# Optimization experiments

Measured on AMD Instinct MI355X. Metric: run time of the kernel, lower is better.

Reference implementation:

```python
import jax, jax.numpy as jnp
import numpy as np

NUM_DAYOFWEEK, NUM_TIME, NUM_MONTH, NUM_DAY = 7, 24, 12, 31
NUM_DESTINATION = 100000
NUM_FACTOR = 128
NUM_DIM = NUM_FACTOR // 4  # 32
N = 1048576


def setup_inputs() -> dict:
    key = jax.random.key(0)
    ks = jax.random.split(key, 10)
    std = 0.1
    return {
        "dayofweek": jax.random.randint(ks[0], (N,), 0, NUM_DAYOFWEEK),
        "time": jax.random.randint(ks[1], (N,), 0, NUM_TIME),
        "month": jax.random.randint(ks[2], (N,), 0, NUM_MONTH),
        "day": jax.random.randint(ks[3], (N,), 0, NUM_DAY),
        "destination": jax.random.randint(ks[4], (N,), 0, NUM_DESTINATION),
        "W_dayofweek": std * jax.random.normal(ks[5], (NUM_DAYOFWEEK, NUM_DIM), dtype=jnp.float32),
        "W_time": std * jax.random.normal(ks[6], (NUM_TIME, NUM_DIM), dtype=jnp.float32),
        "W_month": std * jax.random.normal(ks[7], (NUM_MONTH, NUM_DIM), dtype=jnp.float32),
        "W_day": std * jax.random.normal(ks[8], (NUM_DAY, NUM_DIM), dtype=jnp.float32),
        "W_item": std * jax.random.normal(ks[9], (NUM_DESTINATION, NUM_FACTOR), dtype=jnp.float32),
    }


def reference(dayofweek, time, month, day, destination,
              W_dayofweek, W_time, W_month, W_day, W_item) -> jnp.ndarray:
    # Gather per-feature embeddings and concat into user vector [N, num_factor]
    user = jnp.concatenate([
        W_dayofweek[dayofweek],  # [N, 32]
        W_time[time],            # [N, 32]
        W_month[month],          # [N, 32]
        W_day[day],              # [N, 32]
    ], axis=-1)
    item = W_item[destination]   # [N, 128]
    # Original: diagonal(mm(user, item.T)) == rowwise dot product; compute it directly.
    return jnp.sum(user * item, axis=-1)  # [N]
```

## Files before the change

### kernel.cpp

```cpp
#include <hip/hip_runtime.h>


constexpr int NDIM = 32;
constexpr int SZ_DOW = 7 * NDIM, SZ_TIM = 24 * NDIM, SZ_MON = 12 * NDIM, SZ_DAY = 31 * NDIM;
constexpr int B_DOW = 0;
constexpr int B_TIM = B_DOW + SZ_DOW;
constexpr int B_MON = B_TIM + SZ_TIM;
constexpr int B_DAY = B_MON + SZ_MON;
constexpr int TAB_TOT = B_DAY + SZ_DAY;

constexpr int NB   = 32;
constexpr int DDIV = 3125;
constexpr int NBLK = 256;
constexpr int SPB  = 4096;

typedef unsigned long long u64;

__global__ __launch_bounds__(256)
void bin_kernel(const int* __restrict__ dow, const int* __restrict__ tim,
                const int* __restrict__ mon, const int* __restrict__ day,
                const int* __restrict__ dest,
                int* __restrict__ cntG, int* __restrict__ lbaseG,
                u64* __restrict__ payload, unsigned short* __restrict__ invl, int n)
{
    __shared__ u64 stage[SPB];
    __shared__ unsigned short ist[SPB];
    __shared__ int hist[NB], lbase[NB], cursor[NB];

    const int t = threadIdx.x, b = blockIdx.x;
    const int g0 = b * SPB;
    const int rem = n - g0;
    const int len = rem < SPB ? rem : SPB;

    int dreg[16];
#pragma unroll
    for (int i = 0; i < 16; i++) {
        const int k = i * 256 + t;
        dreg[i] = (k < len) ? dest[g0 + k] : -1;
    }
    if (t < NB) hist[t] = 0;
    __syncthreads();
#pragma unroll
    for (int i = 0; i < 16; i++)
        if (dreg[i] >= 0) atomicAdd(&hist[dreg[i] / DDIV], 1);
    __syncthreads();
    if (t == 0) {
        int run = 0;
        for (int q = 0; q < NB; q++) { lbase[q] = run; run += hist[q]; }
    }
    __syncthreads();
    if (t < NB) { cursor[t] = lbase[t]; cntG[b * NB + t] = hist[t]; lbaseG[b * NB + t] = lbase[t]; }
    __syncthreads();
#pragma unroll
    for (int i = 0; i < 16; i++) {
        const int k = i * 256 + t;
        if (k < len) {
            const int ds = dreg[i];
            const int q  = ds / DDIV;
            const int j  = atomicAdd(&cursor[q], 1);
            const u64 p = (u64)(unsigned)(g0 + k)
                | ((u64)(unsigned)ds          << 20)
                | ((u64)(unsigned)dow[g0 + k] << 37)
                | ((u64)(unsigned)tim[g0 + k] << 40)
                | ((u64)(unsigned)mon[g0 + k] << 45)
                | ((u64)(unsigned)day[g0 + k] << 49);
            stage[j] = p;
            ist[k] = (unsigned short)j;
        }
    }
    __syncthreads();
#pragma unroll
    for (int i = 0; i < 16; i++) {
        const int k = i * 256 + t;
        if (k < len) {
            payload[g0 + k] = stage[k];
            if (invl) invl[g0 + k] = ist[k];
        }
    }
}

__global__ __launch_bounds__(256, 4)
void mf_main_kernel(const u64* __restrict__ payload,
                    const float* __restrict__ Wdow, const float* __restrict__ Wtim,
                    const float* __restrict__ Wmon, const float* __restrict__ Wday,
                    const float* __restrict__ Witem,
                    const int* __restrict__ cntG, const int* __restrict__ lbaseG,
                    float* __restrict__ res, float* __restrict__ out)
{
    __shared__ float tab[TAB_TOT];
    const int tid = threadIdx.x;
    for (int i = tid; i < SZ_DOW; i += 256) tab[B_DOW + i] = Wdow[i];
    for (int i = tid; i < SZ_TIM; i += 256) tab[B_TIM + i] = Wtim[i];
    for (int i = tid; i < SZ_MON; i += 256) tab[B_MON + i] = Wmon[i];
    for (int i = tid; i < SZ_DAY; i += 256) tab[B_DAY + i] = Wday[i];
    __syncthreads();

    const int sub = tid & 63;
    const int wv  = tid >> 6;
    const int g   = sub >> 3;
    const int l8  = sub & 7;
    const int col = l8 * 4;
    const int tb[4] = {B_DOW, B_TIM, B_MON, B_DAY};
    const int sh[4] = {37, 40, 45, 49};
    const int mk[4] = {7, 31, 15, 31};

    const int x = blockIdx.x & 7;
    const int s = blockIdx.x >> 3;

    for (int p = 0; p < 4; p++) {
        const int q  = x + 8 * p;
        const int L  = cntG[s * NB + q];
        const int st = s * SPB + lbaseG[s * NB + q];

        for (int i = wv * 16; i < L; i += 64) {
            const int i0 = i + g, i1 = i + 8 + g;
            const bool v0 = i0 < L, v1 = i1 < L;

            const u64 p0 = v0 ? payload[st + i0] : 0ull;
            const u64 p1 = v1 ? payload[st + i1] : 0ull;

            const int id0 = (int)(p0 & 0xFFFFFull), d0 = (int)((p0 >> 20) & 0x1FFFFull);
            const int id1 = (int)(p1 & 0xFFFFFull), d1 = (int)((p1 >> 20) & 0x1FFFFull);

            const float* r0 = Witem + (long)d0 * 128 + col;
            const float* r1 = Witem + (long)d1 * 128 + col;

            float4 it0[4], it1[4], us0[4], us1[4];
#pragma unroll
            for (int j = 0; j < 4; j++) it0[j] = *reinterpret_cast<const float4*>(r0 + j * NDIM);
#pragma unroll
            for (int j = 0; j < 4; j++) it1[j] = *reinterpret_cast<const float4*>(r1 + j * NDIM);
#pragma unroll
            for (int j = 0; j < 4; j++) {
                const int idx = (int)((p0 >> sh[j]) & (u64)mk[j]);
                us0[j] = *reinterpret_cast<const float4*>(&tab[tb[j] + idx * NDIM + col]);
            }
#pragma unroll
            for (int j = 0; j < 4; j++) {
                const int idx = (int)((p1 >> sh[j]) & (u64)mk[j]);
                us1[j] = *reinterpret_cast<const float4*>(&tab[tb[j] + idx * NDIM + col]);
            }

            float a0 = 0.f, a1 = 0.f;
#pragma unroll
            for (int j = 0; j < 4; j++) {
                a0 += it0[j].x * us0[j].x + it0[j].y * us0[j].y
                    + it0[j].z * us0[j].z + it0[j].w * us0[j].w;
                a1 += it1[j].x * us1[j].x + it1[j].y * us1[j].y
                    + it1[j].z * us1[j].z + it1[j].w * us1[j].w;
            }

            a0 += __shfl_xor(a0, 1);  a1 += __shfl_xor(a1, 1);
            a0 += __shfl_xor(a0, 2);  a1 += __shfl_xor(a1, 2);
            a0 += __shfl_xor(a0, 4);  a1 += __shfl_xor(a1, 4);

            if (l8 == 0) {
                if (res) {
                    if (v0) res[st + i0] = a0;
                    if (v1) res[st + i1] = a1;
                } else {
                    if (v0) out[id0] = a0;
                    if (v1) out[id1] = a1;
                }
            }
        }
    }
}

__global__ __launch_bounds__(256)
void unperm_kernel(const float* __restrict__ res, const unsigned short* __restrict__ invl,
                   float* __restrict__ out, int n)
{
    __shared__ float r[SPB];
    const int t = threadIdx.x, b = blockIdx.x;
    const int g0 = b * SPB;
    const int rem = n - g0;
    const int len = rem < SPB ? rem : SPB;
#pragma unroll
    for (int i = 0; i < 16; i++) {
        const int k = i * 256 + t;
        if (k < len) r[k] = res[g0 + k];
    }
    __syncthreads();
#pragma unroll
    for (int i = 0; i < 16; i++) {
        const int k = i * 256 + t;
        if (k < len) out[g0 + k] = r[invl[g0 + k]];
    }
}

__global__ __launch_bounds__(256, 8)
void mf_dot_kernel(const int* __restrict__ dow, const int* __restrict__ tim,
                   const int* __restrict__ mon, const int* __restrict__ day,
                   const int* __restrict__ dest,
                   const float* __restrict__ Wdow, const float* __restrict__ Wtim,
                   const float* __restrict__ Wmon, const float* __restrict__ Wday,
                   const float* __restrict__ Witem,
                   float* __restrict__ out, int n_samples)
{
    __shared__ float tab[TAB_TOT];
    const int tid = threadIdx.x;
    for (int i = tid; i < SZ_DOW; i += 256) tab[B_DOW + i] = Wdow[i];
    for (int i = tid; i < SZ_TIM; i += 256) tab[B_TIM + i] = Wtim[i];
    for (int i = tid; i < SZ_MON; i += 256) tab[B_MON + i] = Wmon[i];
    for (int i = tid; i < SZ_DAY; i += 256) tab[B_DAY + i] = Wday[i];
    __syncthreads();
    const int lane = tid & 63, sub = lane & 31, wave = tid >> 6, half = lane >> 5;
    const int t = sub >> 3, dofs = (sub & 7) * 4;
    const int* idxp  = (t == 0) ? dow   : (t == 1) ? tim   : (t == 2) ? mon   : day;
    const int  tbase = (t == 0) ? B_DOW : (t == 1) ? B_TIM : (t == 2) ? B_MON : B_DAY;
    long n = (long)blockIdx.x * 8 + wave * 2 + half;
    const long stride = (long)gridDim.x * 8;
    for (; n < n_samples; n += stride) {
        const int idx = idxp[n];
        const int ds  = dest[n];
        const float4 u  = *reinterpret_cast<const float4*>(&tab[tbase + idx * NDIM + dofs]);
        const float4 it = *reinterpret_cast<const float4*>(&Witem[(long)ds * 128 + sub * 4]);
        float r = u.x * it.x + u.y * it.y + u.z * it.z + u.w * it.w;
        r += __shfl_xor(r, 16); r += __shfl_xor(r, 8); r += __shfl_xor(r, 4);
        r += __shfl_xor(r, 2);  r += __shfl_xor(r, 1);
        if (sub == 0) out[n] = r;
    }
}

extern "C" void kernel_launch(void* const* d_in, const int* in_sizes, int n_in,
                              void* d_out, int out_size, void* d_ws, size_t ws_size,
                              hipStream_t stream)
{
    const int*   dow   = (const int*)d_in[0];
    const int*   tim   = (const int*)d_in[1];
    const int*   mon   = (const int*)d_in[2];
    const int*   day   = (const int*)d_in[3];
    const int*   dest  = (const int*)d_in[4];
    const float* Wdow  = (const float*)d_in[5];
    const float* Wtim  = (const float*)d_in[6];
    const float* Wmon  = (const float*)d_in[7];
    const float* Wday  = (const float*)d_in[8];
    const float* Witem = (const float*)d_in[9];
    float* out = (float*)d_out;

    const int n = in_sizes[0];
    const int cap = NBLK * SPB;

    const size_t off_payload = 64 * 1024;
    const size_t off_invl    = off_payload + (size_t)cap * 8;
    const size_t off_res     = off_invl + (size_t)cap * 2;
    const size_t need_full   = off_res + (size_t)cap * 4;
    const size_t need_mid    = off_invl;

    if ((size_t)ws_size < need_mid || n > cap) {
        hipLaunchKernelGGL(mf_dot_kernel, dim3(2048), dim3(256), 0, stream,
                           dow, tim, mon, day, dest,
                           Wdow, Wtim, Wmon, Wday, Witem, out, n);
        return;
    }

    const bool full = (size_t)ws_size >= need_full;

    int* cntG   = (int*)d_ws;
    int* lbaseG = (int*)((char*)d_ws + 32 * 1024);
    u64* payload = (u64*)((char*)d_ws + off_payload);
    unsigned short* invl = full ? (unsigned short*)((char*)d_ws + off_invl) : nullptr;
    float* res           = full ? (float*)((char*)d_ws + off_res) : nullptr;

    hipLaunchKernelGGL(bin_kernel, dim3(NBLK), dim3(256), 0, stream,
                       dow, tim, mon, day, dest, cntG, lbaseG, payload, invl, n);
    hipLaunchKernelGGL(mf_main_kernel, dim3(2048), dim3(256), 0, stream,
                       payload, Wdow, Wtim, Wmon, Wday, Witem, cntG, lbaseG, res, out);
    if (full)
        hipLaunchKernelGGL(unperm_kernel, dim3(NBLK), dim3(256), 0, stream,
                           res, invl, out, n);
}
```

Measured before the change: 167.8 us.

## Halve bin segment size, pad LDS table rows, prefetch indices in bin kernel

Segments shrink from 4096 to 2048 samples, which doubles the bin and unperm block count and gives the main kernel 4096 blocks with higher occupancy bounds. The user-embedding table in LDS is padded to a row stride of 36 floats to reduce bank conflicts on the float4 reads. The bin kernel loads the four small index arrays together with dest and packs them early, instead of loading them inside the atomic scatter loop. The partial-workspace path is removed, so the three-kernel pipeline now needs the full workspace or falls back to the direct kernel. Smaller segments also mean fewer samples per destination bucket and more per-block overhead.

```diff
diff --git a/kernel.cpp b/kernel.cpp
--- a/kernel.cpp
+++ b/kernel.cpp
@@ -2,21 +2,32 @@
 
 
 constexpr int NDIM = 32;
-constexpr int SZ_DOW = 7 * NDIM, SZ_TIM = 24 * NDIM, SZ_MON = 12 * NDIM, SZ_DAY = 31 * NDIM;
+constexpr int TS   = 36;
+constexpr int R_DOW = 7, R_TIM = 24, R_MON = 12, R_DAY = 31;
 constexpr int B_DOW = 0;
-constexpr int B_TIM = B_DOW + SZ_DOW;
-constexpr int B_MON = B_TIM + SZ_TIM;
-constexpr int B_DAY = B_MON + SZ_MON;
-constexpr int TAB_TOT = B_DAY + SZ_DAY;
+constexpr int B_TIM = B_DOW + R_DOW * TS;
+constexpr int B_MON = B_TIM + R_TIM * TS;
+constexpr int B_DAY = B_MON + R_MON * TS;
+constexpr int TAB_TOT = B_DAY + R_DAY * TS;
 
 constexpr int NB   = 32;
 constexpr int DDIV = 3125;
-constexpr int NBLK = 256;
-constexpr int SPB  = 4096;
+constexpr int NBLK = 512;
+constexpr int SPB  = 2048;
+constexpr int IPT  = SPB / 256;
 
 typedef unsigned long long u64;
 
-__global__ __launch_bounds__(256)
+__device__ __forceinline__ void load_tab(float* tab, const float* Wdow, const float* Wtim,
+                                         const float* Wmon, const float* Wday) {
+    const int t = threadIdx.x;
+    for (int i = t; i < R_DOW * NDIM; i += 256) tab[B_DOW + (i >> 5) * TS + (i & 31)] = Wdow[i];
+    for (int i = t; i < R_TIM * NDIM; i += 256) tab[B_TIM + (i >> 5) * TS + (i & 31)] = Wtim[i];
+    for (int i = t; i < R_MON * NDIM; i += 256) tab[B_MON + (i >> 5) * TS + (i & 31)] = Wmon[i];
+    for (int i = t; i < R_DAY * NDIM; i += 256) tab[B_DAY + (i >> 5) * TS + (i & 31)] = Wday[i];
+}
+
+__global__ __launch_bounds__(256, 2)
 void bin_kernel(const int* __restrict__ dow, const int* __restrict__ tim,
                 const int* __restrict__ mon, const int* __restrict__ day,
                 const int* __restrict__ dest,
@@ -32,16 +43,20 @@
     const int rem = n - g0;
     const int len = rem < SPB ? rem : SPB;
 
-    int dreg[16];
-#pragma unroll
-    for (int i = 0; i < 16; i++) {
-        const int k = i * 256 + t;
-        dreg[i] = (k < len) ? dest[g0 + k] : -1;
+    int dreg[IPT], pkreg[IPT];
+#pragma unroll
+    for (int i = 0; i < IPT; i++) {
+        const int k = i * 256 + t;
+        if (k < len) {
+            const int idx = g0 + k;
+            dreg[i]  = dest[idx];
+            pkreg[i] = dow[idx] | (tim[idx] << 3) | (mon[idx] << 8) | (day[idx] << 12);
+        } else { dreg[i] = -1; pkreg[i] = 0; }
     }
     if (t < NB) hist[t] = 0;
     __syncthreads();
 #pragma unroll
-    for (int i = 0; i < 16; i++)
+    for (int i = 0; i < IPT; i++)
         if (dreg[i] >= 0) atomicAdd(&hist[dreg[i] / DDIV], 1);
     __syncthreads();
     if (t == 0) {
@@ -52,49 +67,41 @@
     if (t < NB) { cursor[t] = lbase[t]; cntG[b * NB + t] = hist[t]; lbaseG[b * NB + t] = lbase[t]; }
     __syncthreads();
 #pragma unroll
-    for (int i = 0; i < 16; i++) {
+    for (int i = 0; i < IPT; i++) {
         const int k = i * 256 + t;
         if (k < len) {
             const int ds = dreg[i];
-            const int q  = ds / DDIV;
-            const int j  = atomicAdd(&cursor[q], 1);
-            const u64 p = (u64)(unsigned)(g0 + k)
-                | ((u64)(unsigned)ds          << 20)
-                | ((u64)(unsigned)dow[g0 + k] << 37)
-                | ((u64)(unsigned)tim[g0 + k] << 40)
-                | ((u64)(unsigned)mon[g0 + k] << 45)
-                | ((u64)(unsigned)day[g0 + k] << 49);
-            stage[j] = p;
+            const int j  = atomicAdd(&cursor[ds / DDIV], 1);
+            stage[j] = (u64)(unsigned)(g0 + k)
+                     | ((u64)(unsigned)ds       << 20)
+                     | ((u64)(unsigned)pkreg[i] << 37);
             ist[k] = (unsigned short)j;
         }
     }
     __syncthreads();
 #pragma unroll
-    for (int i = 0; i < 16; i++) {
+    for (int i = 0; i < IPT; i++) {
         const int k = i * 256 + t;
         if (k < len) {
             payload[g0 + k] = stage[k];
-            if (invl) invl[g0 + k] = ist[k];
+            invl[g0 + k]    = ist[k];
         }
     }
 }
 
-__global__ __launch_bounds__(256, 4)
+__global__ __launch_bounds__(256, 8)
 void mf_main_kernel(const u64* __restrict__ payload,
                     const float* __restrict__ Wdow, const float* __restrict__ Wtim,
                     const float* __restrict__ Wmon, const float* __restrict__ Wday,
                     const float* __restrict__ Witem,
                     const int* __restrict__ cntG, const int* __restrict__ lbaseG,
-                    float* __restrict__ res, float* __restrict__ out)
+                    float* __restrict__ res)
 {
     __shared__ float tab[TAB_TOT];
+    load_tab(tab, Wdow, Wtim, Wmon, Wday);
+    __syncthreads();
+
     const int tid = threadIdx.x;
-    for (int i = tid; i < SZ_DOW; i += 256) tab[B_DOW + i] = Wdow[i];
-    for (int i = tid; i < SZ_TIM; i += 256) tab[B_TIM + i] = Wtim[i];
-    for (int i = tid; i < SZ_MON; i += 256) tab[B_MON + i] = Wmon[i];
-    for (int i = tid; i < SZ_DAY; i += 256) tab[B_DAY + i] = Wday[i];
-    __syncthreads();
-
     const int sub = tid & 63;
     const int wv  = tid >> 6;
     const int g   = sub >> 3;
@@ -119,8 +126,8 @@
             const u64 p0 = v0 ? payload[st + i0] : 0ull;
             const u64 p1 = v1 ? payload[st + i1] : 0ull;
 
-            const int id0 = (int)(p0 & 0xFFFFFull), d0 = (int)((p0 >> 20) & 0x1FFFFull);
-            const int id1 = (int)(p1 & 0xFFFFFull), d1 = (int)((p1 >> 20) & 0x1FFFFull);
+            const int d0 = (int)((p0 >> 20) & 0x1FFFFull);
+            const int d1 = (int)((p1 >> 20) & 0x1FFFFull);
 
             const float* r0 = Witem + (long)d0 * 128 + col;
             const float* r1 = Witem + (long)d1 * 128 + col;
@@ -133,12 +140,12 @@
 #pragma unroll
             for (int j = 0; j < 4; j++) {
                 const int idx = (int)((p0 >> sh[j]) & (u64)mk[j]);
-                us0[j] = *reinterpret_cast<const float4*>(&tab[tb[j] + idx * NDIM + col]);
+                us0[j] = *reinterpret_cast<const float4*>(&tab[tb[j] + idx * TS + col]);
             }
 #pragma unroll
             for (int j = 0; j < 4; j++) {
                 const int idx = (int)((p1 >> sh[j]) & (u64)mk[j]);
-                us1[j] = *reinterpret_cast<const float4*>(&tab[tb[j] + idx * NDIM + col]);
+                us1[j] = *reinterpret_cast<const float4*>(&tab[tb[j] + idx * TS + col]);
             }
 
             float a0 = 0.f, a1 = 0.f;
@@ -155,19 +162,14 @@
             a0 += __shfl_xor(a0, 4);  a1 += __shfl_xor(a1, 4);
 
             if (l8 == 0) {
-                if (res) {
-                    if (v0) res[st + i0] = a0;
-                    if (v1) res[st + i1] = a1;
-                } else {
-                    if (v0) out[id0] = a0;
-                    if (v1) out[id1] = a1;
-                }
+                if (v0) res[st + i0] = a0;
+                if (v1) res[st + i1] = a1;
             }
         }
     }
 }
 
-__global__ __launch_bounds__(256)
+__global__ __launch_bounds__(256, 2)
 void unperm_kernel(const float* __restrict__ res, const unsigned short* __restrict__ invl,
                    float* __restrict__ out, int n)
 {
@@ -177,13 +179,13 @@
     const int rem = n - g0;
     const int len = rem < SPB ? rem : SPB;
 #pragma unroll
-    for (int i = 0; i < 16; i++) {
+    for (int i = 0; i < IPT; i++) {
         const int k = i * 256 + t;
         if (k < len) r[k] = res[g0 + k];
     }
     __syncthreads();
 #pragma unroll
-    for (int i = 0; i < 16; i++) {
+    for (int i = 0; i < IPT; i++) {
         const int k = i * 256 + t;
         if (k < len) out[g0 + k] = r[invl[g0 + k]];
     }
@@ -199,12 +201,9 @@
                    float* __restrict__ out, int n_samples)
 {
     __shared__ float tab[TAB_TOT];
+    load_tab(tab, Wdow, Wtim, Wmon, Wday);
+    __syncthreads();
     const int tid = threadIdx.x;
-    for (int i = tid; i < SZ_DOW; i += 256) tab[B_DOW + i] = Wdow[i];
-    for (int i = tid; i < SZ_TIM; i += 256) tab[B_TIM + i] = Wtim[i];
-    for (int i = tid; i < SZ_MON; i += 256) tab[B_MON + i] = Wmon[i];
-    for (int i = tid; i < SZ_DAY; i += 256) tab[B_DAY + i] = Wday[i];
-    __syncthreads();
     const int lane = tid & 63, sub = lane & 31, wave = tid >> 6, half = lane >> 5;
     const int t = sub >> 3, dofs = (sub & 7) * 4;
     const int* idxp  = (t == 0) ? dow   : (t == 1) ? tim   : (t == 2) ? mon   : day;
@@ -214,7 +213,7 @@
     for (; n < n_samples; n += stride) {
         const int idx = idxp[n];
         const int ds  = dest[n];
-        const float4 u  = *reinterpret_cast<const float4*>(&tab[tbase + idx * NDIM + dofs]);
+        const float4 u  = *reinterpret_cast<const float4*>(&tab[tbase + idx * TS + dofs]);
         const float4 it = *reinterpret_cast<const float4*>(&Witem[(long)ds * 128 + sub * 4]);
         float r = u.x * it.x + u.y * it.y + u.z * it.z + u.w * it.w;
         r += __shfl_xor(r, 16); r += __shfl_xor(r, 8); r += __shfl_xor(r, 4);
@@ -242,32 +241,28 @@
     const int n = in_sizes[0];
     const int cap = NBLK * SPB;
 
-    const size_t off_payload = 64 * 1024;
+    const size_t off_payload = 128 * 1024;
     const size_t off_invl    = off_payload + (size_t)cap * 8;
     const size_t off_res     = off_invl + (size_t)cap * 2;
-    const size_t need_full   = off_res + (size_t)cap * 4;
-    const size_t need_mid    = off_invl;
-
-    if ((size_t)ws_size < need_mid || n > cap) {
+    const size_t need        = off_res + (size_t)cap * 4;
+
+    if ((size_t)ws_size < need || n > cap) {
         hipLaunchKernelGGL(mf_dot_kernel, dim3(2048), dim3(256), 0, stream,
                            dow, tim, mon, day, dest,
                            Wdow, Wtim, Wmon, Wday, Witem, out, n);
         return;
     }
 
-    const bool full = (size_t)ws_size >= need_full;
-
-    int* cntG   = (int*)d_ws;
-    int* lbaseG = (int*)((char*)d_ws + 32 * 1024);
+    int* cntG    = (int*)d_ws;
+    int* lbaseG  = (int*)((char*)d_ws + 64 * 1024);
     u64* payload = (u64*)((char*)d_ws + off_payload);
-    unsigned short* invl = full ? (unsigned short*)((char*)d_ws + off_invl) : nullptr;
-    float* res           = full ? (float*)((char*)d_ws + off_res) : nullptr;
+    unsigned short* invl = (unsigned short*)((char*)d_ws + off_invl);
+    float* res           = (float*)((char*)d_ws + off_res);
 
     hipLaunchKernelGGL(bin_kernel, dim3(NBLK), dim3(256), 0, stream,
                        dow, tim, mon, day, dest, cntG, lbaseG, payload, invl, n);
-    hipLaunchKernelGGL(mf_main_kernel, dim3(2048), dim3(256), 0, stream,
-                       payload, Wdow, Wtim, Wmon, Wday, Witem, cntG, lbaseG, res, out);
-    if (full)
-        hipLaunchKernelGGL(unperm_kernel, dim3(NBLK), dim3(256), 0, stream,
-                           res, invl, out, n);
-}
+    hipLaunchKernelGGL(mf_main_kernel, dim3(NBLK * 8), dim3(256), 0, stream,
+                       payload, Wdow, Wtim, Wmon, Wday, Witem, cntG, lbaseG, res);
+    hipLaunchKernelGGL(unperm_kernel, dim3(NBLK), dim3(256), 0, stream,
+                       res, invl, out, n);
+}
```

New measurement: 162.1 us. -3.4%, faster.
